# Optimization experiments

Hardware: AMD Instinct MI355X
Metric: run time of the kernel (lower is better)

Reference implementation:

```python
import jax, jax.numpy as jnp
import numpy as np

N_NODES = 100000
N_EDGES = 3200000
IN_DIM, HD_DIM, OUT_DIM = 512, 256, 128


def spmm(edge_row, edge_col, edge_val, x):
    # y[i] = sum_{e: row[e]=i} val[e] * x[col[e]]  -- sparse adj @ dense x
    msgs = edge_val[:, None] * x[edge_col]          # [E, D]
    return jax.ops.segment_sum(msgs, edge_row, num_segments=N_NODES)


def setup_inputs() -> dict:
    key = jax.random.key(0)
    k1, k2, k3, k4, k5, k6, k7, k8 = jax.random.split(key, 8)
    x = jax.random.normal(k1, (N_NODES, IN_DIM), dtype=jnp.float32)
    edge_row = jax.random.randint(k2, (N_EDGES,), 0, N_NODES, dtype=jnp.int64)
    edge_col = jax.random.randint(k3, (N_EDGES,), 0, N_NODES, dtype=jnp.int64)
    edge_val = jax.random.uniform(k4, (N_EDGES,), dtype=jnp.float32)
    s0 = 1.0 / np.sqrt(IN_DIM)
    s1 = 1.0 / np.sqrt(HD_DIM)
    W0 = jax.random.uniform(k5, (IN_DIM, HD_DIM), dtype=jnp.float32, minval=-s0, maxval=s0)
    b0 = jax.random.uniform(k6, (HD_DIM,), dtype=jnp.float32, minval=-s0, maxval=s0)
    W1 = jax.random.uniform(k7, (HD_DIM, OUT_DIM), dtype=jnp.float32, minval=-s1, maxval=s1)
    b1 = jax.random.uniform(k8, (OUT_DIM,), dtype=jnp.float32, minval=-s1, maxval=s1)
    return {"x": x, "edge_row": edge_row, "edge_col": edge_col, "edge_val": edge_val,
            "W0": W0, "b0": b0, "W1": W1, "b1": b1}


def reference(x, edge_row, edge_col, edge_val, W0, b0, W1, b1):
    # eval mode: dropout is identity
    h = x @ W0 + b0                                  # li0: [N, HD]
    h = spmm(edge_row, edge_col, edge_val, h)        # adj @ h
    h = spmm(edge_row, edge_col, edge_val, h)        # adj @ (adj @ h)
    return jax.nn.relu(h) @ W1 + b1                  # li1(relu(.)): [N, OUT]
```

## Files before the change

kernel.cpp:

```cpp
#include <hip/hip_runtime.h>

#define N_NODES 100000
#define N_EDGES 3200000
#define IN_DIM  512
#define HD_DIM  256
#define OUT_DIM 128

#define NBINS  391
#define BINCAP 9216
#define EPT    16
#define EPB    (256 * EPT)

typedef short   short8  __attribute__((ext_vector_type(8)));
typedef unsigned short ushort8 __attribute__((ext_vector_type(8)));
typedef float   floatx4 __attribute__((ext_vector_type(4)));

__device__ __forceinline__ unsigned short f2bf(float f) {
    unsigned int u = __float_as_uint(f);
    u += 0x7fffu + ((u >> 16) & 1u);
    return (unsigned short)(u >> 16);
}

__device__ __forceinline__ unsigned f2bf_pk(float lo, float hi) {
    unsigned r;
    asm("v_cvt_pk_bf16_f32 %0, %1, %2" : "=v"(r) : "v"(lo), "v"(hi));
    return r;
}


__global__ __launch_bounds__(256) void bin_scatter(const int* __restrict__ erow,
                                                   const int* __restrict__ ecol,
                                                   const float* __restrict__ eval,
                                                   int* __restrict__ gcnt,
                                                   uint2* __restrict__ binned, int E) {
    __shared__ int hist[NBINS];
    __shared__ int sd[512];
    __shared__ int lbase[NBINS];
    __shared__ int gbase[NBINS];
    __shared__ int cur[NBINS];
    __shared__ unsigned short sbin[EPB];
    __shared__ uint2 sedge[EPB];

    const int t = threadIdx.x;
    for (int i = t; i < NBINS; i += 256) hist[i] = 0;
    __syncthreads();

    long base = (long)blockIdx.x * EPB + t * EPT;
    int rows[EPT];
    const bool valid = base < E;
    if (valid) {
        const int4* p = (const int4*)(erow + base);
#pragma unroll
        for (int v = 0; v < 4; v++) {
            int4 r = p[v];
            rows[4 * v + 0] = r.x; rows[4 * v + 1] = r.y;
            rows[4 * v + 2] = r.z; rows[4 * v + 3] = r.w;
        }
#pragma unroll
        for (int u = 0; u < EPT; u++) atomicAdd(&hist[rows[u] >> 8], 1);
    }
    __syncthreads();

    sd[t]       = (t < NBINS) ? hist[t] : 0;
    sd[t + 256] = (t + 256 < NBINS) ? hist[t + 256] : 0;
    __syncthreads();
    for (int off = 1; off < 512; off <<= 1) {
        int a0 = (t >= off) ? sd[t - off] : 0;
        int a1 = (t + 256 >= off) ? sd[t + 256 - off] : 0;
        __syncthreads();
        sd[t] += a0;
        sd[t + 256] += a1;
        __syncthreads();
    }

    for (int i = t; i < NBINS; i += 256) {
        int h  = hist[i];
        int lb = sd[i] - h;
        lbase[i] = lb;
        cur[i]   = lb;
        gbase[i] = h ? (i * BINCAP + atomicAdd(&gcnt[i], h)) : 0;
    }
    __syncthreads();

    if (valid) {
        const int4*   pc = (const int4*)(ecol + base);
        const float4* pv = (const float4*)(eval + base);
#pragma unroll
        for (int v = 0; v < 4; v++) {
            int4 c4 = pc[v];
            float4 v4 = pv[v];
            int   cs[4] = {c4.x, c4.y, c4.z, c4.w};
            float vs[4] = {v4.x, v4.y, v4.z, v4.w};
#pragma unroll
            for (int u = 0; u < 4; u++) {
                int r = rows[4 * v + u];
                int bin = r >> 8;
                int lpos = atomicAdd(&cur[bin], 1);
                sedge[lpos] = make_uint2(((unsigned)(r & 255) << 20) | (unsigned)cs[u],
                                         __float_as_uint(vs[u]));
                sbin[lpos] = (unsigned short)bin;
            }
        }
    }
    __syncthreads();

    const int ns = sd[NBINS - 1];
    for (int i = t; i < ns; i += 256) {
        int bin = sbin[i];
        int gpos = gbase[bin] + (i - lbase[bin]);
        if (gpos < (bin + 1) * BINCAP)
            binned[gpos] = sedge[i];
    }
}

__global__ __launch_bounds__(256) void bin_finalize(const int* __restrict__ gcnt,
                                                    const uint2* __restrict__ binned,
                                                    int* __restrict__ rowptr,
                                                    int* __restrict__ binend,
                                                    uint2* __restrict__ csr) {
    __shared__ int hist[256];
    __shared__ int cur[256];
    __shared__ uint2 stage[BINCAP];
    const int b = blockIdx.x;
    const int t = threadIdx.x;
    int n = gcnt[b];
    if (n > BINCAP) n = BINCAP;
    const int s = b * BINCAP;

    hist[t] = 0;
    __syncthreads();
    for (int i = s + t; i < s + n; i += 256)
        atomicAdd(&hist[binned[i].x >> 20], 1);
    __syncthreads();
    int v = hist[t];
    for (int off = 1; off < 256; off <<= 1) {
        int add = (t >= off) ? hist[t - off] : 0;
        __syncthreads();
        hist[t] += add;
        __syncthreads();
    }
    int excl = hist[t] - v;
    int r = (b << 8) + t;
    if (r <= N_NODES) rowptr[r] = s + excl;
    if (t == 0) binend[b] = s + n;
    cur[t] = excl;
    __syncthreads();
    for (int i = s + t; i < s + n; i += 256) {
        uint2 ev = binned[i];
        int pos = atomicAdd(&cur[ev.x >> 20], 1);
        stage[pos] = make_uint2(ev.x & 0xFFFFFu, ev.y);
    }
    __syncthreads();
    for (int i = t; i < n; i += 256)
        csr[s + i] = stage[i];
}


__global__ void transpose_bf16(const float* __restrict__ in, unsigned short* __restrict__ out,
                               int K, int N) {
    int idx = blockIdx.x * blockDim.x + threadIdx.x;
    if (idx < K * N) {
        int k = idx / N, n = idx - k * N;
        out[n * K + k] = f2bf(in[idx]);
    }
}


template <bool A_FP32, bool RELU_A, bool OUT_BF16, int BN>
__global__ __launch_bounds__(256, 2) void gemm_mfma(const void* __restrict__ Av,
                                                    const unsigned short* __restrict__ BT,
                                                    const float* __restrict__ bias,
                                                    void* __restrict__ Cv,
                                                    int M, int N, int K) {
    constexpr int NJ = BN / 32;
    __shared__ unsigned short As[128 * 40];
    __shared__ unsigned short Bs[BN * 40];
    const int tid  = threadIdx.x;
    const int lane = tid & 63;
    const int wv   = tid >> 6;
    const int wm   = (wv >> 1) * 64;
    const int wn   = (wv & 1) * (BN / 2);
    const int mrow = lane & 15;
    const int q    = lane >> 4;
    const int bm   = blockIdx.x * 128;
    const int bn   = blockIdx.y * BN;

    floatx4 acc[4][NJ] = {};

    const int srow = tid >> 1;
    const int skh  = (tid & 1) * 16;

    for (int k0 = 0; k0 < K; k0 += 32) {
        {
            const int grow = bm + srow;
            if (A_FP32) {
                uint4 w0, w1;
                if (grow < M) {
                    const float* A = (const float*)Av;
                    const float4* p = (const float4*)&A[(long)grow * K + k0 + skh];
                    float4 f;
                    f = p[0]; w0.x = f2bf_pk(f.x, f.y); w0.y = f2bf_pk(f.z, f.w);
                    f = p[1]; w0.z = f2bf_pk(f.x, f.y); w0.w = f2bf_pk(f.z, f.w);
                    f = p[2]; w1.x = f2bf_pk(f.x, f.y); w1.y = f2bf_pk(f.z, f.w);
                    f = p[3]; w1.z = f2bf_pk(f.x, f.y); w1.w = f2bf_pk(f.z, f.w);
                } else {
                    w0 = make_uint4(0, 0, 0, 0);
                    w1 = make_uint4(0, 0, 0, 0);
                }
                *(uint4*)&As[srow * 40 + skh]     = w0;
                *(uint4*)&As[srow * 40 + skh + 8] = w1;
            } else {
                unsigned short tmp[16];
                const unsigned short* A = (const unsigned short*)Av;
                if (grow < M) {
                    const ushort8* p = (const ushort8*)&A[(long)grow * K + k0 + skh];
                    ushort8 u0 = p[0], u1 = p[1];
#pragma unroll
                    for (int v = 0; v < 8; v++) { tmp[v] = u0[v]; tmp[8 + v] = u1[v]; }
                    if (RELU_A) {
#pragma unroll
                        for (int v = 0; v < 16; v++)
                            if (tmp[v] & 0x8000u) tmp[v] = 0;
                    }
                } else {
#pragma unroll
                    for (int v = 0; v < 16; v++) tmp[v] = 0;
                }
                ushort8* dst = (ushort8*)&As[srow * 40 + skh];
                ushort8 w0, w1;
#pragma unroll
                for (int v = 0; v < 8; v++) { w0[v] = tmp[v]; w1[v] = tmp[8 + v]; }
                dst[0] = w0;
                dst[1] = w1;
            }
        }
        if (BN == 128) {
            const int gn = bn + srow;
            const ushort8* p = (const ushort8*)&BT[(long)gn * K + k0 + skh];
            ushort8* dst = (ushort8*)&Bs[srow * 40 + skh];
            dst[0] = p[0];
            dst[1] = p[1];
        } else {
            const int gn = bn + tid;
            const ushort8* p = (const ushort8*)&BT[(long)gn * K + k0];
            ushort8* dst = (ushort8*)&Bs[tid * 40];
            dst[0] = p[0];
            dst[1] = p[1];
            dst[2] = p[2];
            dst[3] = p[3];
        }
        __syncthreads();

        short8 af[4], bf[NJ];
#pragma unroll
        for (int i = 0; i < 4; i++)
            af[i] = *(const short8*)&As[(wm + i * 16 + mrow) * 40 + q * 8];
#pragma unroll
        for (int j = 0; j < NJ; j++)
            bf[j] = *(const short8*)&Bs[(wn + j * 16 + mrow) * 40 + q * 8];
#pragma unroll
        for (int i = 0; i < 4; i++)
#pragma unroll
            for (int j = 0; j < NJ; j++)
                acc[i][j] = __builtin_amdgcn_mfma_f32_16x16x32_bf16(af[i], bf[j], acc[i][j], 0, 0, 0);
        __syncthreads();
    }

#pragma unroll
    for (int i = 0; i < 4; i++) {
#pragma unroll
        for (int r = 0; r < 4; r++) {
            const int row = bm + wm + i * 16 + q * 4 + r;
            if (row < M) {
#pragma unroll
                for (int j = 0; j < NJ; j++) {
                    const int col = bn + wn + j * 16 + mrow;
                    float v = acc[i][j][r] + bias[col];
                    if (OUT_BF16)
                        ((unsigned short*)Cv)[(long)row * N + col] = f2bf(v);
                    else
                        ((float*)Cv)[(long)row * N + col] = v;
                }
            }
        }
    }
}


__global__ __launch_bounds__(256) void spmm_bf16(const int* __restrict__ rowptr,
                                                 const int* __restrict__ binend,
                                                 const uint2* __restrict__ edges,
                                                 const unsigned short* __restrict__ Hin,
                                                 unsigned short* __restrict__ Hout) {
    const int wave = threadIdx.x >> 6;
    const int lane = threadIdx.x & 63;
    const int r = blockIdx.x * 4 + wave;
    if (r >= N_NODES) return;
    const int s = rowptr[r];
    const int e = ((r & 255) == 255) ? binend[r >> 8] : rowptr[r + 1];
    const uint2* __restrict__ Hv = (const uint2*)Hin;
    float a0 = 0.f, a1 = 0.f, a2 = 0.f, a3 = 0.f;

    for (int base = s; base < e; base += 64) {
        int idx = base + lane;
        uint2 ev = (idx < e) ? edges[idx] : make_uint2(0u, 0u);
        int cnt = e - base;
        if (cnt > 64) cnt = 64;
        for (int j0 = 0; j0 < cnt; j0 += 8) {
            uint2 h[8];
            float v[8];
#pragma unroll
            for (int u = 0; u < 8; u++) {
                int   c = __shfl((int)ev.x, j0 + u);
                v[u]    = __uint_as_float((unsigned)__shfl((int)ev.y, j0 + u));
                h[u]    = Hv[((unsigned)c << 6) + lane];
            }
#pragma unroll
            for (int u = 0; u < 8; u++) {
                a0 += v[u] * __uint_as_float(h[u].x << 16);
                a1 += v[u] * __uint_as_float(h[u].x & 0xffff0000u);
                a2 += v[u] * __uint_as_float(h[u].y << 16);
                a3 += v[u] * __uint_as_float(h[u].y & 0xffff0000u);
            }
        }
    }
    uint2 o;
    o.x = (unsigned)f2bf(a0) | ((unsigned)f2bf(a1) << 16);
    o.y = (unsigned)f2bf(a2) | ((unsigned)f2bf(a3) << 16);
    ((uint2*)Hout)[((unsigned)r << 6) + lane] = o;
}


extern "C" void kernel_launch(void* const* d_in, const int* in_sizes, int n_in,
                              void* d_out, int out_size, void* d_ws, size_t ws_size,
                              hipStream_t stream) {
    const float* x    = (const float*)d_in[0];
    const int*   erow = (const int*)d_in[1];
    const int*   ecol = (const int*)d_in[2];
    const float* eval = (const float*)d_in[3];
    const float* W0   = (const float*)d_in[4];
    const float* b0   = (const float*)d_in[5];
    const float* W1   = (const float*)d_in[6];
    const float* b1   = (const float*)d_in[7];
    float* out = (float*)d_out;

    char* ws = (char*)d_ws;
    size_t off = 0;
    auto alloc = [&](size_t bytes) {
        void* p = ws + off;
        off += (bytes + 255) & ~(size_t)255;
        return p;
    };
    int*            rowptr   = (int*)alloc((N_NODES + 1) * sizeof(int));
    int*            gcnt     = (int*)alloc(NBINS * sizeof(int));
    int*            binend   = (int*)alloc(NBINS * sizeof(int));
    uint2*          binned   = (uint2*)alloc((size_t)NBINS * BINCAP * sizeof(uint2));
    uint2*          csr      = (uint2*)alloc((size_t)NBINS * BINCAP * sizeof(uint2));
    unsigned short* W0T      = (unsigned short*)alloc((size_t)IN_DIM * HD_DIM * sizeof(unsigned short));
    unsigned short* W1T      = (unsigned short*)alloc((size_t)HD_DIM * OUT_DIM * sizeof(unsigned short));
    unsigned short* Ha       = (unsigned short*)alloc((size_t)N_NODES * HD_DIM * sizeof(unsigned short));
    unsigned short* Hb       = (unsigned short*)alloc((size_t)N_NODES * HD_DIM * sizeof(unsigned short));

    const int nblk = (N_EDGES + EPB - 1) / EPB;

    hipMemsetAsync(gcnt, 0, NBINS * sizeof(int), stream);
    bin_scatter<<<nblk, 256, 0, stream>>>(erow, ecol, eval, gcnt, binned, N_EDGES);
    bin_finalize<<<NBINS, 256, 0, stream>>>(gcnt, binned, rowptr, binend, csr);

    transpose_bf16<<<(IN_DIM * HD_DIM + 255) / 256, 256, 0, stream>>>(W0, W0T, IN_DIM, HD_DIM);
    transpose_bf16<<<(HD_DIM * OUT_DIM + 255) / 256, 256, 0, stream>>>(W1, W1T, HD_DIM, OUT_DIM);

    gemm_mfma<true, false, true, 256><<<dim3((N_NODES + 127) / 128, HD_DIM / 256), 256, 0, stream>>>(
        x, W0T, b0, Ha, N_NODES, HD_DIM, IN_DIM);

    spmm_bf16<<<(N_NODES + 3) / 4, 256, 0, stream>>>(rowptr, binend, csr, Ha, Hb);
    spmm_bf16<<<(N_NODES + 3) / 4, 256, 0, stream>>>(rowptr, binend, csr, Hb, Ha);

    gemm_mfma<false, true, false, 128><<<dim3((N_NODES + 127) / 128, OUT_DIM / 128), 256, 0, stream>>>(
        Ha, W1T, b1, out, N_NODES, OUT_DIM, HD_DIM);
}
```

Before: 861.8 us.

## Double GEMM K-tile to 64, fuse weight transposes, use nontemporal SpMM accesses

The GEMM kernel now stages a 64-wide K slice per iteration, with a padded LDS stride of 72, and runs two MFMA sub-steps between barriers. This halves the number of sync points and loop iterations, at the cost of more LDS and registers per block. The two weight-transpose launches are merged into one kernel. The SpMM edge loads and output stores now use nontemporal builtins so streaming data does not pollute the cache that holds the gathered feature rows.

```diff
diff --git a/kernel.cpp b/kernel.cpp
--- a/kernel.cpp
+++ b/kernel.cpp
@@ -156,15 +156,23 @@
 }
 
 
-__global__ void transpose_bf16(const float* __restrict__ in, unsigned short* __restrict__ out,
-                               int K, int N) {
+__global__ void transpose_w(const float* __restrict__ W0, unsigned short* __restrict__ W0T,
+                            const float* __restrict__ W1, unsigned short* __restrict__ W1T) {
     int idx = blockIdx.x * blockDim.x + threadIdx.x;
-    if (idx < K * N) {
-        int k = idx / N, n = idx - k * N;
-        out[n * K + k] = f2bf(in[idx]);
-    }
-}
-
+    if (idx < IN_DIM * HD_DIM) {
+        int k = idx / HD_DIM, n = idx - k * HD_DIM;
+        W0T[n * IN_DIM + k] = f2bf(W0[idx]);
+    } else {
+        int j = idx - IN_DIM * HD_DIM;
+        if (j < HD_DIM * OUT_DIM) {
+            int k = j / OUT_DIM, n = j - k * OUT_DIM;
+            W1T[n * HD_DIM + k] = f2bf(W1[j]);
+        }
+    }
+}
+
+
+#define LDW 72
 
 template <bool A_FP32, bool RELU_A, bool OUT_BF16, int BN>
 __global__ __launch_bounds__(256, 2) void gemm_mfma(const void* __restrict__ Av,
@@ -173,8 +181,8 @@
                                                     void* __restrict__ Cv,
                                                     int M, int N, int K) {
     constexpr int NJ = BN / 32;
-    __shared__ unsigned short As[128 * 40];
-    __shared__ unsigned short Bs[BN * 40];
+    __shared__ unsigned short As[128 * LDW];
+    __shared__ unsigned short Bs[BN * LDW];
     const int tid  = threadIdx.x;
     const int lane = tid & 63;
     const int wv   = tid >> 6;
@@ -188,16 +196,16 @@
     floatx4 acc[4][NJ] = {};
 
     const int srow = tid >> 1;
-    const int skh  = (tid & 1) * 16;
-
-    for (int k0 = 0; k0 < K; k0 += 32) {
+    const int sseg = (tid & 1) * 32;
+
+    for (int k0 = 0; k0 < K; k0 += 64) {
         {
             const int grow = bm + srow;
             if (A_FP32) {
                 uint4 w0, w1;
+                const float* A = (const float*)Av;
+                const float4* p = (const float4*)&A[(long)grow * K + k0 + sseg];
                 if (grow < M) {
-                    const float* A = (const float*)Av;
-                    const float4* p = (const float4*)&A[(long)grow * K + k0 + skh];
                     float4 f;
                     f = p[0]; w0.x = f2bf_pk(f.x, f.y); w0.y = f2bf_pk(f.z, f.w);
                     f = p[1]; w0.z = f2bf_pk(f.x, f.y); w0.w = f2bf_pk(f.z, f.w);
@@ -207,62 +215,79 @@
                     w0 = make_uint4(0, 0, 0, 0);
                     w1 = make_uint4(0, 0, 0, 0);
                 }
-                *(uint4*)&As[srow * 40 + skh]     = w0;
-                *(uint4*)&As[srow * 40 + skh + 8] = w1;
+                *(uint4*)&As[srow * LDW + sseg]     = w0;
+                *(uint4*)&As[srow * LDW + sseg + 8] = w1;
+                if (grow < M) {
+                    float4 f;
+                    f = p[4]; w0.x = f2bf_pk(f.x, f.y); w0.y = f2bf_pk(f.z, f.w);
+                    f = p[5]; w0.z = f2bf_pk(f.x, f.y); w0.w = f2bf_pk(f.z, f.w);
+                    f = p[6]; w1.x = f2bf_pk(f.x, f.y); w1.y = f2bf_pk(f.z, f.w);
+                    f = p[7]; w1.z = f2bf_pk(f.x, f.y); w1.w = f2bf_pk(f.z, f.w);
+                }
+                *(uint4*)&As[srow * LDW + sseg + 16] = w0;
+                *(uint4*)&As[srow * LDW + sseg + 24] = w1;
             } else {
-                unsigned short tmp[16];
+                unsigned short tmp[32];
                 const unsigned short* A = (const unsigned short*)Av;
                 if (grow < M) {
-                    const ushort8* p = (const ushort8*)&A[(long)grow * K + k0 + skh];
-                    ushort8 u0 = p[0], u1 = p[1];
-#pragma unroll
-                    for (int v = 0; v < 8; v++) { tmp[v] = u0[v]; tmp[8 + v] = u1[v]; }
+                    const ushort8* p = (const ushort8*)&A[(long)grow * K + k0 + sseg];
+#pragma unroll
+                    for (int v = 0; v < 4; v++) {
+                        ushort8 u = p[v];
+#pragma unroll
+                        for (int j = 0; j < 8; j++) tmp[v * 8 + j] = u[j];
+                    }
                     if (RELU_A) {
 #pragma unroll
-                        for (int v = 0; v < 16; v++)
+                        for (int v = 0; v < 32; v++)
                             if (tmp[v] & 0x8000u) tmp[v] = 0;
                     }
                 } else {
 #pragma unroll
-                    for (int v = 0; v < 16; v++) tmp[v] = 0;
+                    for (int v = 0; v < 32; v++) tmp[v] = 0;
                 }
-                ushort8* dst = (ushort8*)&As[srow * 40 + skh];
-                ushort8 w0, w1;
-#pragma unroll
-                for (int v = 0; v < 8; v++) { w0[v] = tmp[v]; w1[v] = tmp[8 + v]; }
-                dst[0] = w0;
-                dst[1] = w1;
+                ushort8* dst = (ushort8*)&As[srow * LDW + sseg];
+#pragma unroll
+                for (int v = 0; v < 4; v++) {
+                    ushort8 w;
+#pragma unroll
+                    for (int j = 0; j < 8; j++) w[j] = tmp[v * 8 + j];
+                    dst[v] = w;
+                }
             }
         }
         if (BN == 128) {
             const int gn = bn + srow;
-            const ushort8* p = (const ushort8*)&BT[(long)gn * K + k0 + skh];
-            ushort8* dst = (ushort8*)&Bs[srow * 40 + skh];
-            dst[0] = p[0];
-            dst[1] = p[1];
-        } else {
-            const int gn = bn + tid;
-            const ushort8* p = (const ushort8*)&BT[(long)gn * K + k0];
-            ushort8* dst = (ushort8*)&Bs[tid * 40];
+            const ushort8* p = (const ushort8*)&BT[(long)gn * K + k0 + sseg];
+            ushort8* dst = (ushort8*)&Bs[srow * LDW + sseg];
             dst[0] = p[0];
             dst[1] = p[1];
             dst[2] = p[2];
             dst[3] = p[3];
-        }
-        __syncthreads();
-
-        short8 af[4], bf[NJ];
-#pragma unroll
-        for (int i = 0; i < 4; i++)
-            af[i] = *(const short8*)&As[(wm + i * 16 + mrow) * 40 + q * 8];
-#pragma unroll
-        for (int j = 0; j < NJ; j++)
-            bf[j] = *(const short8*)&Bs[(wn + j * 16 + mrow) * 40 + q * 8];
-#pragma unroll
-        for (int i = 0; i < 4; i++)
+        } else {
+            const int gn = bn + tid;
+            const ushort8* p = (const ushort8*)&BT[(long)gn * K + k0];
+            ushort8* dst = (ushort8*)&Bs[tid * LDW];
+#pragma unroll
+            for (int v = 0; v < 8; v++) dst[v] = p[v];
+        }
+        __syncthreads();
+
+#pragma unroll
+        for (int ks = 0; ks < 2; ks++) {
+            short8 af[4], bf[NJ];
+#pragma unroll
+            for (int i = 0; i < 4; i++)
+                af[i] = *(const short8*)&As[(wm + i * 16 + mrow) * LDW + ks * 32 + q * 8];
 #pragma unroll
             for (int j = 0; j < NJ; j++)
-                acc[i][j] = __builtin_amdgcn_mfma_f32_16x16x32_bf16(af[i], bf[j], acc[i][j], 0, 0, 0);
+                bf[j] = *(const short8*)&Bs[(wn + j * 16 + mrow) * LDW + ks * 32 + q * 8];
+#pragma unroll
+            for (int i = 0; i < 4; i++)
+#pragma unroll
+                for (int j = 0; j < NJ; j++)
+                    acc[i][j] = __builtin_amdgcn_mfma_f32_16x16x32_bf16(af[i], bf[j], acc[i][j], 0, 0, 0);
+        }
         __syncthreads();
     }
 
@@ -303,7 +328,13 @@
 
     for (int base = s; base < e; base += 64) {
         int idx = base + lane;
-        uint2 ev = (idx < e) ? edges[idx] : make_uint2(0u, 0u);
+        uint2 ev = make_uint2(0u, 0u);
+        if (idx < e) {
+            unsigned long long raw =
+                __builtin_nontemporal_load((const unsigned long long*)edges + idx);
+            ev.x = (unsigned)raw;
+            ev.y = (unsigned)(raw >> 32);
+        }
         int cnt = e - base;
         if (cnt > 64) cnt = 64;
         for (int j0 = 0; j0 < cnt; j0 += 8) {
@@ -324,10 +355,9 @@
             }
         }
     }
-    uint2 o;
-    o.x = (unsigned)f2bf(a0) | ((unsigned)f2bf(a1) << 16);
-    o.y = (unsigned)f2bf(a2) | ((unsigned)f2bf(a3) << 16);
-    ((uint2*)Hout)[((unsigned)r << 6) + lane] = o;
+    unsigned long long o = (unsigned long long)((unsigned)f2bf(a0) | ((unsigned)f2bf(a1) << 16))
+                         | ((unsigned long long)((unsigned)f2bf(a2) | ((unsigned)f2bf(a3) << 16)) << 32);
+    __builtin_nontemporal_store(o, (unsigned long long*)Hout + (((unsigned)r << 6) + lane));
 }
 
 
@@ -367,8 +397,8 @@
     bin_scatter<<<nblk, 256, 0, stream>>>(erow, ecol, eval, gcnt, binned, N_EDGES);
     bin_finalize<<<NBINS, 256, 0, stream>>>(gcnt, binned, rowptr, binend, csr);
 
-    transpose_bf16<<<(IN_DIM * HD_DIM + 255) / 256, 256, 0, stream>>>(W0, W0T, IN_DIM, HD_DIM);
-    transpose_bf16<<<(HD_DIM * OUT_DIM + 255) / 256, 256, 0, stream>>>(W1, W1T, HD_DIM, OUT_DIM);
+    transpose_w<<<(IN_DIM * HD_DIM + HD_DIM * OUT_DIM + 255) / 256, 256, 0, stream>>>(
+        W0, W0T, W1, W1T);
 
     gemm_mfma<true, false, true, 256><<<dim3((N_NODES + 127) / 128, HD_DIM / 256), 256, 0, stream>>>(
         x, W0T, b0, Ha, N_NODES, HD_DIM, IN_DIM);
```

Result: no change. 870.5 us (+1.0%).
